# Kernel optimization log

Measured on AMD Instinct MI355X. Metric: run time of the kernel, lower is better.

## Reference

```python
import jax, jax.numpy as jnp
import numpy as np

T, B, I, H, L = 512, 64, 1024, 1024, 2


def setup_inputs() -> dict:
    key = jax.random.key(0)
    ks = jax.random.split(key, 10)
    stdv = 1.0 / np.sqrt(H)
    u = lambda k, shape: jax.random.uniform(k, shape, jnp.float32, -stdv, stdv)
    return {
        "x": jax.random.normal(ks[0], (T, B, I), jnp.float32),
        "hx": jnp.zeros((L, B, H), jnp.float32),
        "cx": jnp.zeros((L, B, H), jnp.float32),
        "w_ih0": u(ks[1], (4 * H, I)),
        "w_hh0": u(ks[2], (4 * H, H)),
        "b_ih0": u(ks[3], (4 * H,)),
        "b_hh0": u(ks[4], (4 * H,)),
        "w_ih1": u(ks[5], (4 * H, H)),
        "w_hh1": u(ks[6], (4 * H, H)),
        "b_ih1": u(ks[7], (4 * H,)),
        "b_hh1": u(ks[8], (4 * H,)),
    }


def _lstm_layer(x, h0, c0, w_ih, w_hh, b_ih, b_hh):
    # Precompute input contribution for all timesteps: [T, B, 4H]
    igates = jnp.einsum("tbi,gi->tbg", x, w_ih) + b_ih

    def step(carry, ig_t):
        h, c = carry
        gates = ig_t + h @ w_hh.T + b_hh
        i, f, g, o = jnp.split(gates, 4, axis=-1)
        i = jax.nn.sigmoid(i)
        f = jax.nn.sigmoid(f)
        g = jnp.tanh(g)
        o = jax.nn.sigmoid(o)
        c = f * c + i * g
        h = o * jnp.tanh(c)
        return (h, c), h

    (hT, cT), out = jax.lax.scan(step, (h0, c0), igates)
    return out, hT, cT


def reference(x, hx, cx, w_ih0, w_hh0, b_ih0, b_hh0, w_ih1, w_hh1, b_ih1, b_hh1):
    params = [(w_ih0, w_hh0, b_ih0, b_hh0), (w_ih1, w_hh1, b_ih1, b_hh1)]
    out = x
    h_final, c_final = [], []
    for layer in range(L):
        out, hT, cT = _lstm_layer(out, hx[layer], cx[layer], *params[layer])
        h_final.append(hT)
        c_final.append(cT)
    hn = jnp.stack(h_final)  # [L, B, H]
    cn = jnp.stack(c_final)  # [L, B, H]
    return out, (hn, cn)
```

## Files before the change

kernel.cpp:

```cpp
#include <hip/hip_runtime.h>
#include <hip/hip_bf16.h>
#include <hip/hip_cooperative_groups.h>
#include <cstddef>

namespace cg = cooperative_groups;

typedef short bf16x8 __attribute__((ext_vector_type(8)));
typedef float f32x4 __attribute__((ext_vector_type(4)));

#define T_STEPS 512
#define BATCH   64
#define DIM     1024
#define BD      (BATCH*DIM)
#define XB_ELEMS ((size_t)T_STEPS*BATCH*DIM)
#define IGSLOT  262144
#define FSTRIDE 16

__device__ __forceinline__ float sigmoidf_(float x) { return 1.f / (1.f + __expf(-x)); }
__device__ __forceinline__ float tanhf_(float x)    { return 2.f / (1.f + __expf(-2.f * x)) - 1.f; }
__device__ __forceinline__ unsigned short f2bf(float f) {
    union { float f; unsigned int u; } v; v.f = f;
    unsigned int u = v.u + 0x7fffu + ((v.u >> 16) & 1u);
    return (unsigned short)(u >> 16);
}

__device__ __forceinline__ unsigned long long coh_load8(const void* p) {
    return __hip_atomic_load((const unsigned long long*)p,
                             __ATOMIC_RELAXED, __HIP_MEMORY_SCOPE_AGENT);
}
__device__ __forceinline__ void coh_store8(void* p, unsigned long long v) {
    __hip_atomic_store((unsigned long long*)p, v,
                       __ATOMIC_RELAXED, __HIP_MEMORY_SCOPE_AGENT);
}

__global__ void __launch_bounds__(256, 1)
lstm_fused(const float* __restrict__ x,
           const float* __restrict__ hx,
           const float* __restrict__ cx,
           const float* __restrict__ w_ih0, const float* __restrict__ w_hh0,
           const float* __restrict__ b_ih0, const float* __restrict__ b_hh0,
           const float* __restrict__ w_ih1, const float* __restrict__ w_hh1,
           const float* __restrict__ b_ih1, const float* __restrict__ b_hh1,
           float* __restrict__ out,
           unsigned short* __restrict__ ws)
{
    unsigned short* xb = ws;
    unsigned short* h0 = ws + XB_ELEMS;
    unsigned short* h1 = h0 + 4 * BD;
    float* ig0 = (float*)(h1 + 2 * BD);
    float* ig1 = ig0 + 2 * IGSLOT;
    unsigned* flags = (unsigned*)(ig1 + 2 * IGSLOT);

    const int tid  = threadIdx.x;
    const int lane = tid & 63;
    const int wave = tid >> 6;
    const int bid  = blockIdx.x;
    const int role = bid >> 6;
    const int ug   = bid & 63;
    const int ub   = ug * 16;

    __shared__ __align__(16) unsigned short wB[65536];
    __shared__ __align__(16) unsigned short hstage[64][16];

    {
        const float* wm = (role == 0) ? w_ih0 : (role == 1) ? w_hh0
                        : (role == 2) ? w_ih1 : w_hh1;
        for (int idx = tid; idx < 8192; idx += 256) {
            int l  = idx & 63;
            int kc = (idx >> 6) & 31;
            int n  = idx >> 11;
            int c  = l & 15, kq = l >> 4;
            const float* src = wm + (size_t)(n * DIM + ub + c) * DIM + kc * 32 + kq * 8;
            float4 v0 = *(const float4*)(src);
            float4 v1 = *(const float4*)(src + 4);
            unsigned short o[8];
            o[0]=f2bf(v0.x); o[1]=f2bf(v0.y); o[2]=f2bf(v0.z); o[3]=f2bf(v0.w);
            o[4]=f2bf(v1.x); o[5]=f2bf(v1.y); o[6]=f2bf(v1.z); o[7]=f2bf(v1.w);
            *(bf16x8*)(&wB[(size_t)idx * 8]) = *(const bf16x8*)o;
        }
    }

    {
        const int nthr = 256 * gridDim.x;
        const int gtid = bid * 256 + tid;
        const float4* xv = (const float4*)x;
        const int n4 = (int)(XB_ELEMS / 4);
        for (int i = gtid; i < n4; i += nthr) {
            float4 v = xv[i];
            ushort4 o;
            o.x=f2bf(v.x); o.y=f2bf(v.y); o.z=f2bf(v.z); o.w=f2bf(v.w);
            *(ushort4*)(xb + (size_t)i * 4) = o;
        }
    }

    if (role == 1 || role == 3) {
        unsigned short* hdst = (role == 1) ? (h0 + 3 * BD) : (h1 + 1 * BD);
        const float* hsrc = hx + (size_t)(role >> 1) * BD;
        const int kcp = ub >> 5, sub = ub & 31;
        for (int e = tid; e < 1024; e += 256) {
            int row = e >> 4, uu = e & 15;
            hdst[kcp * 2048 + row * 32 + sub + uu] = f2bf(hsrc[row * DIM + ub + uu]);
        }
    }

    if (tid == 0)
        __hip_atomic_store(flags + (size_t)((role << 6) | ug) * FSTRIDE, 0u,
                           __ATOMIC_RELAXED, __HIP_MEMORY_SCOPE_AGENT);

    const int col  = lane & 15;
    const int quad = lane >> 4;

    float biasv[4] = {0.f, 0.f, 0.f, 0.f};
    if (role == 0 || role == 2) {
        const float* bi = (role == 0) ? b_ih0 : b_ih1;
        const float* bh = (role == 0) ? b_hh0 : b_hh1;
        #pragma unroll
        for (int n = 0; n < 4; ++n) {
            int row = n * DIM + ub + col;
            biasv[n] = bi[row] + bh[row];
        }
    }

    float creg[4] = {0.f, 0.f, 0.f, 0.f};
    if (role == 1 || role == 3) {
        const float* csrc = cx + (size_t)(role >> 1) * BD;
        #pragma unroll
        for (int r = 0; r < 4; ++r) {
            int m = wave * 16 + quad * 4 + r;
            creg[r] = csrc[m * DIM + ub + col];
        }
    }

    cg::grid_group grid = cg::this_grid();
    __syncthreads();
    grid.sync();

    const int arow = wave * 16 + col;

    auto poll_ge = [&](const unsigned* f, int target) {
        while ((int)__hip_atomic_load(f, __ATOMIC_RELAXED, __HIP_MEMORY_SCOPE_AGENT) < target)
            __builtin_amdgcn_s_sleep(1);
    };
    auto Fp = [&](int set, int idx) -> unsigned* {
        return flags + (size_t)((set << 6) | idx) * FSTRIDE;
    };
    auto publish = [&](int set, int idx, int val) {
        __hip_atomic_store(Fp(set, idx), (unsigned)val,
                           __ATOMIC_RELAXED, __HIP_MEMORY_SCOPE_AGENT);
    };

    auto gemm_plain = [&](const unsigned short* Ap,
                          f32x4& A0, f32x4& A1, f32x4& A2, f32x4& A3) {
        const unsigned short* Abase = Ap + (size_t)arow * DIM + quad * 8;
        #pragma unroll 8
        for (int kc = 0; kc < 32; ++kc) {
            bf16x8 a  = *(const bf16x8*)(Abase + kc * 32);
            bf16x8 b0 = *(const bf16x8*)(&wB[((size_t)(0*32 + kc)*64 + lane)*8]);
            bf16x8 b1 = *(const bf16x8*)(&wB[((size_t)(1*32 + kc)*64 + lane)*8]);
            bf16x8 b2 = *(const bf16x8*)(&wB[((size_t)(2*32 + kc)*64 + lane)*8]);
            bf16x8 b3 = *(const bf16x8*)(&wB[((size_t)(3*32 + kc)*64 + lane)*8]);
            A0 = __builtin_amdgcn_mfma_f32_16x16x32_bf16(a, b0, A0, 0, 0, 0);
            A1 = __builtin_amdgcn_mfma_f32_16x16x32_bf16(a, b1, A1, 0, 0, 0);
            A2 = __builtin_amdgcn_mfma_f32_16x16x32_bf16(a, b2, A2, 0, 0, 0);
            A3 = __builtin_amdgcn_mfma_f32_16x16x32_bf16(a, b3, A3, 0, 0, 0);
        }
    };

    auto gemm_coh = [&](const unsigned short* Ap, const float* igb,
                        f32x4& A0, f32x4& A1, f32x4& A2, f32x4& A3) {
        const unsigned short* Abase = Ap + (size_t)arow * 32 + quad * 8;
        if (igb) {
            union { f32x4 v; unsigned long long q[2]; } g0, g1, g2, g3;
            g0.q[0] = coh_load8(igb + 0*128); g0.q[1] = coh_load8(igb + 1*128);
            g1.q[0] = coh_load8(igb + 2*128); g1.q[1] = coh_load8(igb + 3*128);
            g2.q[0] = coh_load8(igb + 4*128); g2.q[1] = coh_load8(igb + 5*128);
            g3.q[0] = coh_load8(igb + 6*128); g3.q[1] = coh_load8(igb + 7*128);
            A0 = g0.v; A1 = g1.v; A2 = g2.v; A3 = g3.v;
        }
        union U { bf16x8 v; unsigned long long q[2]; };
        U pre[8];
        #pragma unroll
        for (int i = 0; i < 8; ++i) {
            pre[i].q[0] = coh_load8(Abase + (size_t)i * 2048);
            pre[i].q[1] = coh_load8(Abase + (size_t)i * 2048 + 4);
        }
        #pragma unroll
        for (int kc = 0; kc < 32; ++kc) {
            U cur = pre[kc & 7];
            if (kc < 24) {
                pre[kc & 7].q[0] = coh_load8(Abase + (size_t)(kc + 8) * 2048);
                pre[kc & 7].q[1] = coh_load8(Abase + (size_t)(kc + 8) * 2048 + 4);
            }
            bf16x8 b0 = *(const bf16x8*)(&wB[((size_t)(0*32 + kc)*64 + lane)*8]);
            bf16x8 b1 = *(const bf16x8*)(&wB[((size_t)(1*32 + kc)*64 + lane)*8]);
            bf16x8 b2 = *(const bf16x8*)(&wB[((size_t)(2*32 + kc)*64 + lane)*8]);
            bf16x8 b3 = *(const bf16x8*)(&wB[((size_t)(3*32 + kc)*64 + lane)*8]);
            A0 = __builtin_amdgcn_mfma_f32_16x16x32_bf16(cur.v, b0, A0, 0, 0, 0);
            A1 = __builtin_amdgcn_mfma_f32_16x16x32_bf16(cur.v, b1, A1, 0, 0, 0);
            A2 = __builtin_amdgcn_mfma_f32_16x16x32_bf16(cur.v, b2, A2, 0, 0, 0);
            A3 = __builtin_amdgcn_mfma_f32_16x16x32_bf16(cur.v, b3, A3, 0, 0, 0);
        }
    };

    auto dump_ig = [&](float* slot, int set, int t,
                       f32x4 A0, f32x4 A1, f32x4 A2, f32x4 A3) {
        float* base = slot + (size_t)ug * 4096 + (size_t)wave * 1024 + lane * 2;
        union { f32x4 v; unsigned long long q[2]; } u0, u1, u2, u3;
        u0.v = A0; u1.v = A1; u2.v = A2; u3.v = A3;
        coh_store8(base + 0*128, u0.q[0]); coh_store8(base + 1*128, u0.q[1]);
        coh_store8(base + 2*128, u1.q[0]); coh_store8(base + 3*128, u1.q[1]);
        coh_store8(base + 4*128, u2.q[0]); coh_store8(base + 5*128, u2.q[1]);
        coh_store8(base + 6*128, u3.q[0]); coh_store8(base + 7*128, u3.q[1]);
        asm volatile("s_waitcnt vmcnt(0)" ::: "memory");
        __syncthreads();
        if (tid == 0) publish(set, ug, t + 1);
    };

    const int kcp = ub >> 5, sub = ub & 31;

    for (int t = 0; t < T_STEPS; ++t) {
        f32x4 A0, A1, A2, A3;

        if (role == 0) {
            if (tid == 0) poll_ge(Fp(1, ug), t - 1);
            __syncthreads();
            A0 = f32x4{biasv[0], biasv[0], biasv[0], biasv[0]};
            A1 = f32x4{biasv[1], biasv[1], biasv[1], biasv[1]};
            A2 = f32x4{biasv[2], biasv[2], biasv[2], biasv[2]};
            A3 = f32x4{biasv[3], biasv[3], biasv[3], biasv[3]};
            gemm_plain(xb + (size_t)t * BD, A0, A1, A2, A3);
            dump_ig(ig0 + (size_t)(t & 1) * IGSLOT, 0, t, A0, A1, A2, A3);

        } else if (role == 2) {
            if (tid < 64) poll_ge(Fp(1, tid), t + 1);
            else if (tid == 64) poll_ge(Fp(3, ug), t - 1);
            __syncthreads();
            A0 = f32x4{biasv[0], biasv[0], biasv[0], biasv[0]};
            A1 = f32x4{biasv[1], biasv[1], biasv[1], biasv[1]};
            A2 = f32x4{biasv[2], biasv[2], biasv[2], biasv[2]};
            A3 = f32x4{biasv[3], biasv[3], biasv[3], biasv[3]};
            gemm_coh(h0 + (size_t)(t & 3) * BD, nullptr, A0, A1, A2, A3);
            dump_ig(ig1 + (size_t)(t & 1) * IGSLOT, 2, t, A0, A1, A2, A3);

        } else {
            if (role == 1) {
                if (tid < 64) poll_ge(Fp(1, tid), t);
                else if (tid < 128) poll_ge(Fp(2, tid - 64), t - 3);
                else if (tid == 128) poll_ge(Fp(0, ug), t + 1);
            } else {
                if (tid < 64) poll_ge(Fp(3, tid), t);
                else if (tid == 64) poll_ge(Fp(2, ug), t + 1);
            }
            __syncthreads();

            unsigned short* hring = (role == 1) ? h0 : h1;
            const unsigned short* hsrc = (role == 1)
                ? (h0 + (size_t)((t - 1) & 3) * BD)
                : (h1 + (size_t)((t - 1) & 1) * BD);
            const float* igb = ((role == 1) ? ig0 : ig1) + (size_t)(t & 1) * IGSLOT
                             + (size_t)ug * 4096 + (size_t)wave * 1024 + lane * 2;
            gemm_coh(hsrc, igb, A0, A1, A2, A3);

            float hreg[4];
            #pragma unroll
            for (int r = 0; r < 4; ++r) {
                float ig_ = sigmoidf_(A0[r]);
                float fg_ = sigmoidf_(A1[r]);
                float gg_ = tanhf_(A2[r]);
                float og_ = sigmoidf_(A3[r]);
                float c   = fg_ * creg[r] + ig_ * gg_;
                creg[r]   = c;
                float h   = og_ * tanhf_(c);
                hreg[r]   = h;
                int m = wave * 16 + quad * 4 + r;
                hstage[m][col] = f2bf(h);
            }
            __syncthreads();
            unsigned short* hout = hring
                + (size_t)((role == 1) ? (t & 3) : (t & 1)) * BD;
            if (wave == 0) {
                const unsigned long long* src = (const unsigned long long*)&hstage[lane][0];
                unsigned long long v0 = src[0], v1 = src[1], v2 = src[2], v3 = src[3];
                unsigned short* dst = hout + (size_t)kcp * 2048 + (size_t)lane * 32 + sub;
                coh_store8(dst + 0,  v0);
                coh_store8(dst + 4,  v1);
                coh_store8(dst + 8,  v2);
                coh_store8(dst + 12, v3);
                asm volatile("s_waitcnt vmcnt(0)" ::: "memory");
                if (tid == 0) publish(role, ug, t + 1);
            }

            if (role == 3) {
                #pragma unroll
                for (int r = 0; r < 4; ++r) {
                    int m = wave * 16 + quad * 4 + r;
                    out[(size_t)t * BD + (size_t)m * DIM + ub + col] = hreg[r];
                    if (t == T_STEPS - 1) {
                        out[(size_t)T_STEPS * BD + 1 * BD + m * DIM + ub + col] = hreg[r];
                        out[(size_t)T_STEPS * BD + 3 * BD + m * DIM + ub + col] = creg[r];
                    }
                }
            } else if (t == T_STEPS - 1) {
                #pragma unroll
                for (int r = 0; r < 4; ++r) {
                    int m = wave * 16 + quad * 4 + r;
                    out[(size_t)T_STEPS * BD + 0 * BD + m * DIM + ub + col] = hreg[r];
                    out[(size_t)T_STEPS * BD + 2 * BD + m * DIM + ub + col] = creg[r];
                }
            }
        }
    }
}

extern "C" void kernel_launch(void* const* d_in, const int* in_sizes, int n_in,
                              void* d_out, int out_size, void* d_ws, size_t ws_size,
                              hipStream_t stream) {
    const float* x     = (const float*)d_in[0];
    const float* hx    = (const float*)d_in[1];
    const float* cx    = (const float*)d_in[2];
    const float* w_ih0 = (const float*)d_in[3];
    const float* w_hh0 = (const float*)d_in[4];
    const float* b_ih0 = (const float*)d_in[5];
    const float* b_hh0 = (const float*)d_in[6];
    const float* w_ih1 = (const float*)d_in[7];
    const float* w_hh1 = (const float*)d_in[8];
    const float* b_ih1 = (const float*)d_in[9];
    const float* b_hh1 = (const float*)d_in[10];
    float* outp = (float*)d_out;
    unsigned short* wsp = (unsigned short*)d_ws;

    void* args[] = { &x, &hx, &cx, &w_ih0, &w_hh0, &b_ih0, &b_hh0,
                     &w_ih1, &w_hh1, &b_ih1, &b_hh1, &outp, &wsp };
    hipLaunchCooperativeKernel((void*)lstm_fused, dim3(256), dim3(256),
                               args, 0, stream);
}
```

Measured before the change: 4.006 ms.

## Split the K dimension across two wave groups with an LDS reduction

Doubles the block size to 512 threads, so each of the four row waves gets a partner wave. Each pair splits the 1024-wide K loop into two halves, and the partials are summed through a shared-memory buffer. Only the first half of the waves applies the bias, gate activations and output stores. The aim is to shorten the serial MFMA and load chain on the latency-bound recurrent step, at the cost of an extra barrier and an LDS round trip per step.

```diff
diff --git a/kernel.cpp b/kernel.cpp
--- a/kernel.cpp
+++ b/kernel.cpp
@@ -33,7 +33,7 @@
                        __ATOMIC_RELAXED, __HIP_MEMORY_SCOPE_AGENT);
 }
 
-__global__ void __launch_bounds__(256, 1)
+__global__ void __launch_bounds__(512, 2)
 lstm_fused(const float* __restrict__ x,
            const float* __restrict__ hx,
            const float* __restrict__ cx,
@@ -54,6 +54,8 @@
     const int tid  = threadIdx.x;
     const int lane = tid & 63;
     const int wave = tid >> 6;
+    const int kw   = wave >> 2;
+    const int mw   = wave & 3;
     const int bid  = blockIdx.x;
     const int role = bid >> 6;
     const int ug   = bid & 63;
@@ -61,11 +63,12 @@
 
     __shared__ __align__(16) unsigned short wB[65536];
     __shared__ __align__(16) unsigned short hstage[64][16];
+    __shared__ __align__(16) f32x4 red[4][4][64];
 
     {
         const float* wm = (role == 0) ? w_ih0 : (role == 1) ? w_hh0
                         : (role == 2) ? w_ih1 : w_hh1;
-        for (int idx = tid; idx < 8192; idx += 256) {
+        for (int idx = tid; idx < 8192; idx += 512) {
             int l  = idx & 63;
             int kc = (idx >> 6) & 31;
             int n  = idx >> 11;
@@ -81,8 +84,8 @@
     }
 
     {
-        const int nthr = 256 * gridDim.x;
-        const int gtid = bid * 256 + tid;
+        const int nthr = 512 * gridDim.x;
+        const int gtid = bid * 512 + tid;
         const float4* xv = (const float4*)x;
         const int n4 = (int)(XB_ELEMS / 4);
         for (int i = gtid; i < n4; i += nthr) {
@@ -96,10 +99,10 @@
     if (role == 1 || role == 3) {
         unsigned short* hdst = (role == 1) ? (h0 + 3 * BD) : (h1 + 1 * BD);
         const float* hsrc = hx + (size_t)(role >> 1) * BD;
-        const int kcp = ub >> 5, sub = ub & 31;
-        for (int e = tid; e < 1024; e += 256) {
+        const int kcp0 = ub >> 5, sub0 = ub & 31;
+        for (int e = tid; e < 1024; e += 512) {
             int row = e >> 4, uu = e & 15;
-            hdst[kcp * 2048 + row * 32 + sub + uu] = f2bf(hsrc[row * DIM + ub + uu]);
+            hdst[kcp0 * 2048 + row * 32 + sub0 + uu] = f2bf(hsrc[row * DIM + ub + uu]);
         }
     }
 
@@ -111,7 +114,7 @@
     const int quad = lane >> 4;
 
     float biasv[4] = {0.f, 0.f, 0.f, 0.f};
-    if (role == 0 || role == 2) {
+    if ((role == 0 || role == 2) && kw == 0) {
         const float* bi = (role == 0) ? b_ih0 : b_ih1;
         const float* bh = (role == 0) ? b_hh0 : b_hh1;
         #pragma unroll
@@ -122,11 +125,11 @@
     }
 
     float creg[4] = {0.f, 0.f, 0.f, 0.f};
-    if (role == 1 || role == 3) {
+    if ((role == 1 || role == 3) && kw == 0) {
         const float* csrc = cx + (size_t)(role >> 1) * BD;
         #pragma unroll
         for (int r = 0; r < 4; ++r) {
-            int m = wave * 16 + quad * 4 + r;
+            int m = mw * 16 + quad * 4 + r;
             creg[r] = csrc[m * DIM + ub + col];
         }
     }
@@ -135,7 +138,8 @@
     __syncthreads();
     grid.sync();
 
-    const int arow = wave * 16 + col;
+    const int arow = mw * 16 + col;
+    const int kc0  = kw * 16;
 
     auto poll_ge = [&](const unsigned* f, int target) {
         while ((int)__hip_atomic_load(f, __ATOMIC_RELAXED, __HIP_MEMORY_SCOPE_AGENT) < target)
@@ -151,10 +155,11 @@
 
     auto gemm_plain = [&](const unsigned short* Ap,
                           f32x4& A0, f32x4& A1, f32x4& A2, f32x4& A3) {
-        const unsigned short* Abase = Ap + (size_t)arow * DIM + quad * 8;
+        const unsigned short* Abase = Ap + (size_t)arow * DIM + quad * 8 + kc0 * 32;
         #pragma unroll 8
-        for (int kc = 0; kc < 32; ++kc) {
-            bf16x8 a  = *(const bf16x8*)(Abase + kc * 32);
+        for (int k2 = 0; k2 < 16; ++k2) {
+            int kc = kc0 + k2;
+            bf16x8 a  = *(const bf16x8*)(Abase + k2 * 32);
             bf16x8 b0 = *(const bf16x8*)(&wB[((size_t)(0*32 + kc)*64 + lane)*8]);
             bf16x8 b1 = *(const bf16x8*)(&wB[((size_t)(1*32 + kc)*64 + lane)*8]);
             bf16x8 b2 = *(const bf16x8*)(&wB[((size_t)(2*32 + kc)*64 + lane)*8]);
@@ -168,7 +173,8 @@
 
     auto gemm_coh = [&](const unsigned short* Ap, const float* igb,
                         f32x4& A0, f32x4& A1, f32x4& A2, f32x4& A3) {
-        const unsigned short* Abase = Ap + (size_t)arow * 32 + quad * 8;
+        const unsigned short* Abase = Ap + (size_t)arow * 32 + quad * 8
+                                    + (size_t)kc0 * 2048;
         if (igb) {
             union { f32x4 v; unsigned long long q[2]; } g0, g1, g2, g3;
             g0.q[0] = coh_load8(igb + 0*128); g0.q[1] = coh_load8(igb + 1*128);
@@ -185,12 +191,13 @@
             pre[i].q[1] = coh_load8(Abase + (size_t)i * 2048 + 4);
         }
         #pragma unroll
-        for (int kc = 0; kc < 32; ++kc) {
-            U cur = pre[kc & 7];
-            if (kc < 24) {
-                pre[kc & 7].q[0] = coh_load8(Abase + (size_t)(kc + 8) * 2048);
-                pre[kc & 7].q[1] = coh_load8(Abase + (size_t)(kc + 8) * 2048 + 4);
-            }
+        for (int k2 = 0; k2 < 16; ++k2) {
+            U cur = pre[k2 & 7];
+            if (k2 < 8) {
+                pre[k2 & 7].q[0] = coh_load8(Abase + (size_t)(k2 + 8) * 2048);
+                pre[k2 & 7].q[1] = coh_load8(Abase + (size_t)(k2 + 8) * 2048 + 4);
+            }
+            int kc = kc0 + k2;
             bf16x8 b0 = *(const bf16x8*)(&wB[((size_t)(0*32 + kc)*64 + lane)*8]);
             bf16x8 b1 = *(const bf16x8*)(&wB[((size_t)(1*32 + kc)*64 + lane)*8]);
             bf16x8 b2 = *(const bf16x8*)(&wB[((size_t)(2*32 + kc)*64 + lane)*8]);
@@ -202,15 +209,29 @@
         }
     };
 
+    auto k_reduce = [&](f32x4& A0, f32x4& A1, f32x4& A2, f32x4& A3) {
+        if (kw) {
+            red[0][mw][lane] = A0; red[1][mw][lane] = A1;
+            red[2][mw][lane] = A2; red[3][mw][lane] = A3;
+        }
+        __syncthreads();
+        if (!kw) {
+            A0 += red[0][mw][lane]; A1 += red[1][mw][lane];
+            A2 += red[2][mw][lane]; A3 += red[3][mw][lane];
+        }
+    };
+
     auto dump_ig = [&](float* slot, int set, int t,
                        f32x4 A0, f32x4 A1, f32x4 A2, f32x4 A3) {
-        float* base = slot + (size_t)ug * 4096 + (size_t)wave * 1024 + lane * 2;
-        union { f32x4 v; unsigned long long q[2]; } u0, u1, u2, u3;
-        u0.v = A0; u1.v = A1; u2.v = A2; u3.v = A3;
-        coh_store8(base + 0*128, u0.q[0]); coh_store8(base + 1*128, u0.q[1]);
-        coh_store8(base + 2*128, u1.q[0]); coh_store8(base + 3*128, u1.q[1]);
-        coh_store8(base + 4*128, u2.q[0]); coh_store8(base + 5*128, u2.q[1]);
-        coh_store8(base + 6*128, u3.q[0]); coh_store8(base + 7*128, u3.q[1]);
+        if (!kw) {
+            float* base = slot + (size_t)ug * 4096 + (size_t)mw * 1024 + lane * 2;
+            union { f32x4 v; unsigned long long q[2]; } u0, u1, u2, u3;
+            u0.v = A0; u1.v = A1; u2.v = A2; u3.v = A3;
+            coh_store8(base + 0*128, u0.q[0]); coh_store8(base + 1*128, u0.q[1]);
+            coh_store8(base + 2*128, u1.q[0]); coh_store8(base + 3*128, u1.q[1]);
+            coh_store8(base + 4*128, u2.q[0]); coh_store8(base + 5*128, u2.q[1]);
+            coh_store8(base + 6*128, u3.q[0]); coh_store8(base + 7*128, u3.q[1]);
+        }
         asm volatile("s_waitcnt vmcnt(0)" ::: "memory");
         __syncthreads();
         if (tid == 0) publish(set, ug, t + 1);
@@ -219,27 +240,33 @@
     const int kcp = ub >> 5, sub = ub & 31;
 
     for (int t = 0; t < T_STEPS; ++t) {
-        f32x4 A0, A1, A2, A3;
+        f32x4 A0 = {0,0,0,0}, A1 = {0,0,0,0}, A2 = {0,0,0,0}, A3 = {0,0,0,0};
 
         if (role == 0) {
             if (tid == 0) poll_ge(Fp(1, ug), t - 1);
             __syncthreads();
-            A0 = f32x4{biasv[0], biasv[0], biasv[0], biasv[0]};
-            A1 = f32x4{biasv[1], biasv[1], biasv[1], biasv[1]};
-            A2 = f32x4{biasv[2], biasv[2], biasv[2], biasv[2]};
-            A3 = f32x4{biasv[3], biasv[3], biasv[3], biasv[3]};
+            if (!kw) {
+                A0 = f32x4{biasv[0], biasv[0], biasv[0], biasv[0]};
+                A1 = f32x4{biasv[1], biasv[1], biasv[1], biasv[1]};
+                A2 = f32x4{biasv[2], biasv[2], biasv[2], biasv[2]};
+                A3 = f32x4{biasv[3], biasv[3], biasv[3], biasv[3]};
+            }
             gemm_plain(xb + (size_t)t * BD, A0, A1, A2, A3);
+            k_reduce(A0, A1, A2, A3);
             dump_ig(ig0 + (size_t)(t & 1) * IGSLOT, 0, t, A0, A1, A2, A3);
 
         } else if (role == 2) {
             if (tid < 64) poll_ge(Fp(1, tid), t + 1);
             else if (tid == 64) poll_ge(Fp(3, ug), t - 1);
             __syncthreads();
-            A0 = f32x4{biasv[0], biasv[0], biasv[0], biasv[0]};
-            A1 = f32x4{biasv[1], biasv[1], biasv[1], biasv[1]};
-            A2 = f32x4{biasv[2], biasv[2], biasv[2], biasv[2]};
-            A3 = f32x4{biasv[3], biasv[3], biasv[3], biasv[3]};
+            if (!kw) {
+                A0 = f32x4{biasv[0], biasv[0], biasv[0], biasv[0]};
+                A1 = f32x4{biasv[1], biasv[1], biasv[1], biasv[1]};
+                A2 = f32x4{biasv[2], biasv[2], biasv[2], biasv[2]};
+                A3 = f32x4{biasv[3], biasv[3], biasv[3], biasv[3]};
+            }
             gemm_coh(h0 + (size_t)(t & 3) * BD, nullptr, A0, A1, A2, A3);
+            k_reduce(A0, A1, A2, A3);
             dump_ig(ig1 + (size_t)(t & 1) * IGSLOT, 2, t, A0, A1, A2, A3);
 
         } else {
@@ -257,23 +284,28 @@
             const unsigned short* hsrc = (role == 1)
                 ? (h0 + (size_t)((t - 1) & 3) * BD)
                 : (h1 + (size_t)((t - 1) & 1) * BD);
-            const float* igb = ((role == 1) ? ig0 : ig1) + (size_t)(t & 1) * IGSLOT
-                             + (size_t)ug * 4096 + (size_t)wave * 1024 + lane * 2;
+            const float* igb = (!kw)
+                ? ((role == 1) ? ig0 : ig1) + (size_t)(t & 1) * IGSLOT
+                  + (size_t)ug * 4096 + (size_t)mw * 1024 + lane * 2
+                : nullptr;
             gemm_coh(hsrc, igb, A0, A1, A2, A3);
-
-            float hreg[4];
-            #pragma unroll
-            for (int r = 0; r < 4; ++r) {
-                float ig_ = sigmoidf_(A0[r]);
-                float fg_ = sigmoidf_(A1[r]);
-                float gg_ = tanhf_(A2[r]);
-                float og_ = sigmoidf_(A3[r]);
-                float c   = fg_ * creg[r] + ig_ * gg_;
-                creg[r]   = c;
-                float h   = og_ * tanhf_(c);
-                hreg[r]   = h;
-                int m = wave * 16 + quad * 4 + r;
-                hstage[m][col] = f2bf(h);
+            k_reduce(A0, A1, A2, A3);
+
+            float hreg[4] = {0.f, 0.f, 0.f, 0.f};
+            if (!kw) {
+                #pragma unroll
+                for (int r = 0; r < 4; ++r) {
+                    float ig_ = sigmoidf_(A0[r]);
+                    float fg_ = sigmoidf_(A1[r]);
+                    float gg_ = tanhf_(A2[r]);
+                    float og_ = sigmoidf_(A3[r]);
+                    float c   = fg_ * creg[r] + ig_ * gg_;
+                    creg[r]   = c;
+                    float h   = og_ * tanhf_(c);
+                    hreg[r]   = h;
+                    int m = mw * 16 + quad * 4 + r;
+                    hstage[m][col] = f2bf(h);
+                }
             }
             __syncthreads();
             unsigned short* hout = hring
@@ -290,22 +322,24 @@
                 if (tid == 0) publish(role, ug, t + 1);
             }
 
-            if (role == 3) {
-                #pragma unroll
-                for (int r = 0; r < 4; ++r) {
-                    int m = wave * 16 + quad * 4 + r;
-                    out[(size_t)t * BD + (size_t)m * DIM + ub + col] = hreg[r];
-                    if (t == T_STEPS - 1) {
-                        out[(size_t)T_STEPS * BD + 1 * BD + m * DIM + ub + col] = hreg[r];
-                        out[(size_t)T_STEPS * BD + 3 * BD + m * DIM + ub + col] = creg[r];
+            if (!kw) {
+                if (role == 3) {
+                    #pragma unroll
+                    for (int r = 0; r < 4; ++r) {
+                        int m = mw * 16 + quad * 4 + r;
+                        out[(size_t)t * BD + (size_t)m * DIM + ub + col] = hreg[r];
+                        if (t == T_STEPS - 1) {
+                            out[(size_t)T_STEPS * BD + 1 * BD + m * DIM + ub + col] = hreg[r];
+                            out[(size_t)T_STEPS * BD + 3 * BD + m * DIM + ub + col] = creg[r];
+                        }
                     }
-                }
-            } else if (t == T_STEPS - 1) {
-                #pragma unroll
-                for (int r = 0; r < 4; ++r) {
-                    int m = wave * 16 + quad * 4 + r;
-                    out[(size_t)T_STEPS * BD + 0 * BD + m * DIM + ub + col] = hreg[r];
-                    out[(size_t)T_STEPS * BD + 2 * BD + m * DIM + ub + col] = creg[r];
+                } else if (t == T_STEPS - 1) {
+                    #pragma unroll
+                    for (int r = 0; r < 4; ++r) {
+                        int m = mw * 16 + quad * 4 + r;
+                        out[(size_t)T_STEPS * BD + 0 * BD + m * DIM + ub + col] = hreg[r];
+                        out[(size_t)T_STEPS * BD + 2 * BD + m * DIM + ub + col] = creg[r];
+                    }
                 }
             }
         }
@@ -331,6 +365,6 @@
 
     void* args[] = { &x, &hx, &cx, &w_ih0, &w_hh0, &b_ih0, &b_hh0,
                      &w_ih1, &w_hh1, &b_ih1, &b_hh1, &outp, &wsp };
-    hipLaunchCooperativeKernel((void*)lstm_fused, dim3(256), dim3(256),
+    hipLaunchCooperativeKernel((void*)lstm_fused, dim3(256), dim3(512),
                                args, 0, stream);
 }
```

Measured after the change: 3.548 ms (median of 2 runs). 1.13x faster.
